# Kernel tuning notes

Measured on AMD Instinct MI355X. Metric: run time of the kernel, lower is better.

The kernel has to match this reference:

```python
import jax, jax.numpy as jnp
import numpy as np

N = 100_000   # num nodes
E = 1_600_000 # num edges (before self-loops)
IN = 128      # in_channels (FEATURE_DIM)
H = 64        # hidden_channels (HIDDEN_DIM)
NEG_SLOPE = 0.2


def setup_inputs() -> dict:
    key = jax.random.key(0)
    ks = jax.random.split(key, 8)
    s = 0.05
    return {
        "x": jax.random.normal(ks[0], (N, IN), jnp.float32),
        "edge_index": jax.random.randint(ks[1], (2, E), 0, N, jnp.int32),
        "W_gat": jax.random.normal(ks[2], (IN, H), jnp.float32) * s,
        "att_src": jax.random.normal(ks[3], (H,), jnp.float32) * s,
        "att_dst": jax.random.normal(ks[4], (H,), jnp.float32) * s,
        "b_gat": jnp.zeros((H,), jnp.float32),
        "W1": jax.random.normal(ks[5], (H, H), jnp.float32) * s,
        "b1": jnp.zeros((H,), jnp.float32),
        "W2": jax.random.normal(ks[6], (H, H), jnp.float32) * s,
        "b2": jnp.zeros((H,), jnp.float32),
    }


def _add_self_loops(src, dst, n):
    loop = jnp.arange(n, dtype=src.dtype)
    return jnp.concatenate([src, loop]), jnp.concatenate([dst, loop])


def _segment_softmax(e, seg, n):
    # numerically stable softmax over edges grouped by target node
    m = jax.ops.segment_max(e, seg, num_segments=n)
    m = jnp.where(jnp.isfinite(m), m, 0.0)  # empty segments
    ex = jnp.exp(e - m[seg])
    s = jax.ops.segment_sum(ex, seg, num_segments=n)
    return ex / (s[seg] + 1e-16)


def gat_conv(x, W, a_src, a_dst, b, src, dst, n):
    # PyG GATConv, heads=1: h = xW; e_ij = LeakyReLU(a_s.h_j + a_d.h_i)
    h = x @ W                                   # [N,H]
    alpha_s = h @ a_src                         # [N]
    alpha_d = h @ a_dst                         # [N]
    e = jax.nn.leaky_relu(alpha_s[src] + alpha_d[dst], NEG_SLOPE)  # [E]
    alpha = _segment_softmax(e, dst, n)         # [E]
    out = jax.ops.segment_sum(alpha[:, None] * h[src], dst, num_segments=n)
    return out + b


def gcn_conv(x, W, b, src, dst, n):
    # PyG GCNConv: symmetric normalization D^-1/2 A D^-1/2 (self-loops already added)
    h = x @ W                                   # [N,H]
    deg = jax.ops.segment_sum(jnp.ones(src.shape, h.dtype), dst, num_segments=n)
    dinv = jnp.where(deg > 0, jax.lax.rsqrt(deg), 0.0)
    norm = dinv[src] * dinv[dst]                # [E]
    out = jax.ops.segment_sum(norm[:, None] * h[src], dst, num_segments=n)
    return out + b


def reference(x, edge_index, W_gat, att_src, att_dst, b_gat, W1, b1, W2, b2):
    n = x.shape[0]
    src, dst = _add_self_loops(edge_index[0], edge_index[1], n)
    h = jax.nn.relu(gat_conv(x, W_gat, att_src, att_dst, b_gat, src, dst, n))
    h = jax.nn.relu(gcn_conv(h, W1, b1, src, dst, n))
    h = gcn_conv(h, W2, b2, src, dst, n)
    return h
```

## Files before the change

kernel.cpp:

```cpp
#include <hip/hip_runtime.h>
#include <hip/hip_bf16.h>
#include <math.h>

#define IN_CH 128
#define H_CH  64
#define PBLK  256
#define PTHR  512
#define BKT   256
#define MAXBK 400

typedef __attribute__((ext_vector_type(8))) short bf16x8;
typedef __attribute__((ext_vector_type(4))) float f32x4;


__device__ inline float bflo(unsigned u) { return __uint_as_float(u << 16); }
__device__ inline float bfhi(unsigned u) { return __uint_as_float(u & 0xffff0000u); }
__device__ inline unsigned short f2bf(float f) {
    unsigned x = __float_as_uint(f);
    return (unsigned short)((x + 0x7fffu + ((x >> 16) & 1u)) >> 16);
}
__device__ inline bf16x8 pack8(float4 lo, float4 hi) {
    union { bf16x8 v; unsigned short u[8]; } r;
    r.u[0] = f2bf(lo.x); r.u[1] = f2bf(lo.y); r.u[2] = f2bf(lo.z); r.u[3] = f2bf(lo.w);
    r.u[4] = f2bf(hi.x); r.u[5] = f2bf(hi.y); r.u[6] = f2bf(hi.z); r.u[7] = f2bf(hi.w);
    return r.v;
}
__device__ inline float dot8(float4 a0, float4 a1, float4 b0, float4 b1) {
    return a0.x * b0.x + a0.y * b0.y + a0.z * b0.z + a0.w * b0.w
         + a1.x * b1.x + a1.y * b1.y + a1.z * b1.z + a1.w * b1.w;
}


__global__ __launch_bounds__(PTHR) void passA(const int* __restrict__ ei, int E, int n,
                                              int nbk, int* __restrict__ blkhist) {
    __shared__ int hist[MAXBK];
    int tot = E + n;
    int CH = (tot + gridDim.x - 1) / gridDim.x;
    int beg = blockIdx.x * CH, end = min(tot, beg + CH);
    for (int k = threadIdx.x; k < nbk; k += blockDim.x) hist[k] = 0;
    __syncthreads();
    for (int idx = beg + threadIdx.x; idx < end; idx += blockDim.x) {
        int d = (idx < E) ? ei[E + idx] : (idx - E);
        atomicAdd(&hist[d >> 8], 1);
    }
    __syncthreads();
    for (int k = threadIdx.x; k < nbk; k += blockDim.x)
        blkhist[(size_t)blockIdx.x * nbk + k] = hist[k];
}

__global__ __launch_bounds__(PBLK) void passB1(const int* __restrict__ blkhist,
                                               int* __restrict__ blkbase,
                                               int* __restrict__ btot, int nbk) {
    __shared__ int sh[PBLK];
    int k = blockIdx.x, t = threadIdx.x;
    int v = blkhist[(size_t)t * nbk + k];
    sh[t] = v;
    __syncthreads();
    for (int off = 1; off < PBLK; off <<= 1) {
        int x = (t >= off) ? sh[t - off] : 0;
        __syncthreads();
        sh[t] += x;
        __syncthreads();
    }
    blkbase[(size_t)t * nbk + k] = sh[t] - v;
    if (t == PBLK - 1) btot[k] = sh[PBLK - 1];
}

__global__ __launch_bounds__(512) void passB2(const int* __restrict__ btot,
                                              int* __restrict__ bbase, int nbk, int tot) {
    __shared__ int sh[512];
    int t = threadIdx.x;
    int v = (t < nbk) ? btot[t] : 0;
    sh[t] = v;
    __syncthreads();
    for (int off = 1; off < 512; off <<= 1) {
        int x = (t >= off) ? sh[t - off] : 0;
        __syncthreads();
        sh[t] += x;
        __syncthreads();
    }
    if (t < nbk) bbase[t] = sh[t] - v;
    if (t == 0) bbase[nbk] = tot;
}

__global__ __launch_bounds__(PTHR) void passC(const int* __restrict__ ei, int E, int n, int nbk,
                                              const int* __restrict__ bbase,
                                              const int* __restrict__ blkbase,
                                              int2* __restrict__ pairs) {
    __shared__ int cur[MAXBK];
    int tot = E + n;
    int CH = (tot + gridDim.x - 1) / gridDim.x;
    int beg = blockIdx.x * CH, end = min(tot, beg + CH);
    for (int k = threadIdx.x; k < nbk; k += blockDim.x)
        cur[k] = bbase[k] + blkbase[(size_t)blockIdx.x * nbk + k];
    __syncthreads();
    for (int idx = beg + threadIdx.x; idx < end; idx += blockDim.x) {
        int s, d;
        if (idx < E) { s = ei[idx]; d = ei[E + idx]; }
        else         { s = idx - E; d = idx - E; }
        int pos = atomicAdd(&cur[d >> 8], 1);
        pairs[pos] = make_int2(s, d);
    }
}

__global__ __launch_bounds__(BKT) void passD(const int2* __restrict__ pairs,
                                             const int* __restrict__ bbase, int n, int nbk, int EP,
                                             int* __restrict__ esrc, int* __restrict__ offsets,
                                             float* __restrict__ dinv) {
    __shared__ int cnt[BKT];
    __shared__ int sh[BKT];
    __shared__ int cur[BKT];
    int k = blockIdx.x;
    int nbeg = k << 8;
    int t = threadIdx.x;
    int ebeg = bbase[k], eend = bbase[k + 1];
    cnt[t] = 0;
    __syncthreads();
    for (int e = ebeg + t; e < eend; e += BKT) {
        int2 p = pairs[e];
        atomicAdd(&cnt[p.y - nbeg], 1);
    }
    __syncthreads();
    int v = cnt[t];
    sh[t] = v;
    __syncthreads();
    for (int off = 1; off < BKT; off <<= 1) {
        int x = (t >= off) ? sh[t - off] : 0;
        __syncthreads();
        sh[t] += x;
        __syncthreads();
    }
    int lp = sh[t] - v;
    cur[t] = lp;
    int gn = nbeg + t;
    if (gn < n) {
        offsets[gn] = ebeg + lp;
        dinv[gn] = rsqrtf((float)v);
    }
    __syncthreads();
    for (int e = ebeg + t; e < eend; e += BKT) {
        int2 p = pairs[e];
        int pos = ebeg + atomicAdd(&cur[p.y - nbeg], 1);
        esrc[pos] = p.x;
    }
    if (k == 0 && t == 0) offsets[n] = EP;
}


__global__ void wprep(const float* __restrict__ W, const float* __restrict__ as,
                      const float* __restrict__ ad, float* __restrict__ w_as,
                      float* __restrict__ w_ad, int K) {
    int k = blockIdx.x * blockDim.x + threadIdx.x;
    if (k < K) {
        float s = 0.f, d = 0.f;
        for (int c = 0; c < H_CH; c++) {
            float w = W[(size_t)k * H_CH + c];
            s += w * as[c];
            d += w * ad[c];
        }
        w_as[k] = s;
        w_ad[k] = d;
    }
}


template <int K, bool GAT, bool OUTBF, bool BIASF, typename TIN>
__global__ __launch_bounds__(256) void mfma_gemm(const TIN* __restrict__ X,
                                                 const float* __restrict__ W,
                                                 void* __restrict__ outv,
                                                 const float* __restrict__ w_as,
                                                 const float* __restrict__ w_ad,
                                                 float* __restrict__ alpha_s,
                                                 float* __restrict__ alpha_d,
                                                 const float* __restrict__ bias, int n) {
    constexpr int KF = K / 32;
    int lane = threadIdx.x & 63;
    int wid  = threadIdx.x >> 6;
    int col  = lane & 15;
    int grp  = lane >> 4;

    bf16x8 bfr[KF][4];
#pragma unroll
    for (int kf = 0; kf < KF; kf++) {
        int kb = 32 * kf + 8 * grp;
#pragma unroll
        for (int cf = 0; cf < 4; cf++) {
            float w0[8];
#pragma unroll
            for (int e = 0; e < 8; e++)
                w0[e] = W[(size_t)(kb + e) * H_CH + 16 * cf + col];
            bfr[kf][cf] = pack8(make_float4(w0[0], w0[1], w0[2], w0[3]),
                                make_float4(w0[4], w0[5], w0[6], w0[7]));
        }
    }
    float bb[4] = {0.f, 0.f, 0.f, 0.f};
    if (BIASF) {
#pragma unroll
        for (int cf = 0; cf < 4; cf++) bb[cf] = bias[16 * cf + col];
    }

    int gw = blockIdx.x * (blockDim.x >> 6) + wid;
    int nw = gridDim.x * (blockDim.x >> 6);
    int ns = (n + 15) >> 4;
    for (int s = gw; s < ns; s += nw) {
        int r0 = s << 4;
        int r  = r0 + col;
        const TIN* xr = X + (size_t)(r < n ? r : 0) * K;
        bf16x8 afr[KF];
        float ps = 0.f, pd = 0.f;
#pragma unroll
        for (int kf = 0; kf < KF; kf++) {
            int kb = 32 * kf + 8 * grp;
            if constexpr (sizeof(TIN) == 2) {
                afr[kf] = *(const bf16x8*)(xr + kb);
            } else {
                float4 x0 = *(const float4*)(xr + kb);
                float4 x1 = *(const float4*)(xr + kb + 4);
                if (GAT) {
                    float4 s0 = *(const float4*)(w_as + kb);
                    float4 s1 = *(const float4*)(w_as + kb + 4);
                    float4 d0 = *(const float4*)(w_ad + kb);
                    float4 d1 = *(const float4*)(w_ad + kb + 4);
                    ps += dot8(x0, x1, s0, s1);
                    pd += dot8(x0, x1, d0, d1);
                }
                afr[kf] = pack8(x0, x1);
            }
        }
        f32x4 acc[4];
#pragma unroll
        for (int cf = 0; cf < 4; cf++) {
            acc[cf] = (f32x4){0.f, 0.f, 0.f, 0.f};
#pragma unroll
            for (int kf = 0; kf < KF; kf++)
                acc[cf] = __builtin_amdgcn_mfma_f32_16x16x32_bf16(afr[kf], bfr[kf][cf],
                                                                  acc[cf], 0, 0, 0);
        }
#pragma unroll
        for (int cf = 0; cf < 4; cf++) {
            int cc = 16 * cf + col;
#pragma unroll
            for (int g = 0; g < 4; g++) {
                int rr = r0 + 4 * grp + g;
                if (rr < n) {
                    float v = acc[cf][g] + bb[cf];
                    if (OUTBF) ((unsigned short*)outv)[(size_t)rr * H_CH + cc] = f2bf(v);
                    else       ((float*)outv)[(size_t)rr * H_CH + cc] = v;
                }
            }
        }
        if (GAT) {
            ps += __shfl_xor(ps, 16, 64); ps += __shfl_xor(ps, 32, 64);
            pd += __shfl_xor(pd, 16, 64); pd += __shfl_xor(pd, 32, 64);
            if (grp == 0 && r < n) { alpha_s[r] = ps; alpha_d[r] = pd; }
        }
    }
}


__global__ __launch_bounds__(256) void gat_gather(const unsigned short* __restrict__ h,
                                                  const int* __restrict__ offs,
                                                  const int* __restrict__ esrc,
                                                  const float* __restrict__ as,
                                                  const float* __restrict__ ad,
                                                  const float* __restrict__ bias,
                                                  unsigned short* __restrict__ out, int n) {
    __shared__ int2 sh[4][64];
    int lane = threadIdx.x & 63;
    int wid  = threadIdx.x >> 6;
    int q = lane >> 4, c = lane & 15;
    int gw = (blockIdx.x * blockDim.x + threadIdx.x) >> 6;
    int nw = (gridDim.x * blockDim.x) >> 6;
    float4 bv = *(const float4*)(bias + 4 * c);
    for (int i = gw; i < n; i += nw) {
        int beg = offs[i], end = offs[i + 1];
        float adi = ad[i];
        float a0 = 0.f, a1 = 0.f, a2 = 0.f, a3 = 0.f, s = 0.f;
        for (int base = beg; base < end; base += 64) {
            int l = base + lane;
            int sj = 0; float p = 0.f;
            if (l < end) {
                sj = esrc[l];
                float a = as[sj] + adi;
                float ev = a > 0.f ? a : 0.2f * a;
                p = __expf(ev);
            }
            sh[wid][lane] = make_int2(sj, __float_as_int(p));
            int cnt = min(64, end - base);
            int k = 0;
            for (; k + 16 <= cnt; k += 16) {
                int2 t0 = sh[wid][k + q];
                int2 t1 = sh[wid][k + 4 + q];
                int2 t2 = sh[wid][k + 8 + q];
                int2 t3 = sh[wid][k + 12 + q];
                float p0 = __int_as_float(t0.y), p1 = __int_as_float(t1.y);
                float p2 = __int_as_float(t2.y), p3 = __int_as_float(t3.y);
                uint2 u0 = *(const uint2*)(h + (size_t)t0.x * H_CH + 4 * c);
                uint2 u1 = *(const uint2*)(h + (size_t)t1.x * H_CH + 4 * c);
                uint2 u2 = *(const uint2*)(h + (size_t)t2.x * H_CH + 4 * c);
                uint2 u3 = *(const uint2*)(h + (size_t)t3.x * H_CH + 4 * c);
                a0 += p0 * bflo(u0.x); a1 += p0 * bfhi(u0.x);
                a2 += p0 * bflo(u0.y); a3 += p0 * bfhi(u0.y);
                a0 += p1 * bflo(u1.x); a1 += p1 * bfhi(u1.x);
                a2 += p1 * bflo(u1.y); a3 += p1 * bfhi(u1.y);
                a0 += p2 * bflo(u2.x); a1 += p2 * bfhi(u2.x);
                a2 += p2 * bflo(u2.y); a3 += p2 * bfhi(u2.y);
                a0 += p3 * bflo(u3.x); a1 += p3 * bfhi(u3.x);
                a2 += p3 * bflo(u3.y); a3 += p3 * bfhi(u3.y);
                s += p0 + p1 + p2 + p3;
            }
            for (; k < cnt; k += 4) {
                int2 t0 = sh[wid][k + q];
                float p0 = __int_as_float(t0.y);
                uint2 u0 = *(const uint2*)(h + (size_t)t0.x * H_CH + 4 * c);
                a0 += p0 * bflo(u0.x); a1 += p0 * bfhi(u0.x);
                a2 += p0 * bflo(u0.y); a3 += p0 * bfhi(u0.y);
                s += p0;
            }
        }
        a0 += __shfl_xor(a0, 16, 64); a0 += __shfl_xor(a0, 32, 64);
        a1 += __shfl_xor(a1, 16, 64); a1 += __shfl_xor(a1, 32, 64);
        a2 += __shfl_xor(a2, 16, 64); a2 += __shfl_xor(a2, 32, 64);
        a3 += __shfl_xor(a3, 16, 64); a3 += __shfl_xor(a3, 32, 64);
        s  += __shfl_xor(s, 16, 64);  s  += __shfl_xor(s, 32, 64);
        float invs = 1.f / (s + 1e-16f);
        if (q == 0) {
            ushort4 o;
            o.x = f2bf(fmaxf(a0 * invs + bv.x, 0.f));
            o.y = f2bf(fmaxf(a1 * invs + bv.y, 0.f));
            o.z = f2bf(fmaxf(a2 * invs + bv.z, 0.f));
            o.w = f2bf(fmaxf(a3 * invs + bv.w, 0.f));
            *(ushort4*)(out + (size_t)i * H_CH + 4 * c) = o;
        }
    }
}


template <bool RELU, bool BIASF>
__global__ __launch_bounds__(256) void gcn_gather(const unsigned short* __restrict__ h,
                                                  const int* __restrict__ offs,
                                                  const int* __restrict__ esrc,
                                                  const float* __restrict__ dinv,
                                                  const float* __restrict__ bias,
                                                  unsigned short* __restrict__ out, int n) {
    __shared__ int2 sh[4][64];
    int lane = threadIdx.x & 63;
    int wid  = threadIdx.x >> 6;
    int q = lane >> 4, c = lane & 15;
    int gw = (blockIdx.x * blockDim.x + threadIdx.x) >> 6;
    int nw = (gridDim.x * blockDim.x) >> 6;
    float4 bv = make_float4(0.f, 0.f, 0.f, 0.f);
    if (BIASF) bv = *(const float4*)(bias + 4 * c);
    for (int i = gw; i < n; i += nw) {
        int beg = offs[i], end = offs[i + 1];
        float a0 = 0.f, a1 = 0.f, a2 = 0.f, a3 = 0.f;
        for (int base = beg; base < end; base += 64) {
            int l = base + lane;
            int sj = 0; float wl = 0.f;
            if (l < end) { sj = esrc[l]; wl = dinv[sj]; }
            sh[wid][lane] = make_int2(sj, __float_as_int(wl));
            int cnt = min(64, end - base);
            int k = 0;
            for (; k + 16 <= cnt; k += 16) {
                int2 t0 = sh[wid][k + q];
                int2 t1 = sh[wid][k + 4 + q];
                int2 t2 = sh[wid][k + 8 + q];
                int2 t3 = sh[wid][k + 12 + q];
                float p0 = __int_as_float(t0.y), p1 = __int_as_float(t1.y);
                float p2 = __int_as_float(t2.y), p3 = __int_as_float(t3.y);
                uint2 u0 = *(const uint2*)(h + (size_t)t0.x * H_CH + 4 * c);
                uint2 u1 = *(const uint2*)(h + (size_t)t1.x * H_CH + 4 * c);
                uint2 u2 = *(const uint2*)(h + (size_t)t2.x * H_CH + 4 * c);
                uint2 u3 = *(const uint2*)(h + (size_t)t3.x * H_CH + 4 * c);
                a0 += p0 * bflo(u0.x); a1 += p0 * bfhi(u0.x);
                a2 += p0 * bflo(u0.y); a3 += p0 * bfhi(u0.y);
                a0 += p1 * bflo(u1.x); a1 += p1 * bfhi(u1.x);
                a2 += p1 * bflo(u1.y); a3 += p1 * bfhi(u1.y);
                a0 += p2 * bflo(u2.x); a1 += p2 * bfhi(u2.x);
                a2 += p2 * bflo(u2.y); a3 += p2 * bfhi(u2.y);
                a0 += p3 * bflo(u3.x); a1 += p3 * bfhi(u3.x);
                a2 += p3 * bflo(u3.y); a3 += p3 * bfhi(u3.y);
            }
            for (; k < cnt; k += 4) {
                int2 t0 = sh[wid][k + q];
                float p0 = __int_as_float(t0.y);
                uint2 u0 = *(const uint2*)(h + (size_t)t0.x * H_CH + 4 * c);
                a0 += p0 * bflo(u0.x); a1 += p0 * bfhi(u0.x);
                a2 += p0 * bflo(u0.y); a3 += p0 * bfhi(u0.y);
            }
        }
        a0 += __shfl_xor(a0, 16, 64); a0 += __shfl_xor(a0, 32, 64);
        a1 += __shfl_xor(a1, 16, 64); a1 += __shfl_xor(a1, 32, 64);
        a2 += __shfl_xor(a2, 16, 64); a2 += __shfl_xor(a2, 32, 64);
        a3 += __shfl_xor(a3, 16, 64); a3 += __shfl_xor(a3, 32, 64);
        float di = dinv[i];
        if (q == 0) {
            float v0 = a0 * di + bv.x, v1 = a1 * di + bv.y;
            float v2 = a2 * di + bv.z, v3 = a3 * di + bv.w;
            if (RELU) {
                v0 = fmaxf(v0, 0.f); v1 = fmaxf(v1, 0.f);
                v2 = fmaxf(v2, 0.f); v3 = fmaxf(v3, 0.f);
            }
            ushort4 o;
            o.x = f2bf(v0); o.y = f2bf(v1); o.z = f2bf(v2); o.w = f2bf(v3);
            *(ushort4*)(out + (size_t)i * H_CH + 4 * c) = o;
        }
    }
}


extern "C" void kernel_launch(void* const* d_in, const int* in_sizes, int n_in,
                              void* d_out, int out_size, void* d_ws, size_t ws_size,
                              hipStream_t stream) {
    const float* x       = (const float*)d_in[0];
    const int*   ei      = (const int*)d_in[1];
    const float* W_gat   = (const float*)d_in[2];
    const float* att_src = (const float*)d_in[3];
    const float* att_dst = (const float*)d_in[4];
    const float* b_gat   = (const float*)d_in[5];
    const float* W1      = (const float*)d_in[6];
    const float* b1      = (const float*)d_in[7];
    const float* W2      = (const float*)d_in[8];
    const float* b2      = (const float*)d_in[9];
    float* out = (float*)d_out;

    const int N  = in_sizes[0] / IN_CH;
    const int E  = in_sizes[1] / 2;
    const int EP = E + N;
    const int NBK = (N + BKT - 1) / BKT;

    char* p = (char*)d_ws;
    auto alloc = [&](size_t bytes) -> void* {
        void* r = (void*)p;
        p += (bytes + 255) & ~(size_t)255;
        return r;
    };
    unsigned short* hbf  = (unsigned short*)alloc((size_t)N * H_CH * 2);
    unsigned short* hbfA = (unsigned short*)alloc((size_t)N * H_CH * 2);
    unsigned short* hbf2 = (unsigned short*)alloc((size_t)N * H_CH * 2);
    float* alpha_s = (float*)alloc((size_t)N * 4);
    float* alpha_d = (float*)alloc((size_t)N * 4);
    float* dinv    = (float*)alloc((size_t)N * 4);
    float* w_as_g  = (float*)alloc((size_t)IN_CH * 4);
    float* w_ad_g  = (float*)alloc((size_t)IN_CH * 4);
    int*   offsets = (int*)alloc((size_t)(N + 1) * 4);
    int*   esrc    = (int*)alloc((size_t)EP * 4);
    int2*  pairs   = (int2*)alloc((size_t)EP * 8);
    int*   blkhist = (int*)alloc((size_t)PBLK * NBK * 4);
    int*   blkbase = (int*)alloc((size_t)PBLK * NBK * 4);
    int*   btot    = (int*)alloc((size_t)(NBK + 1) * 4);
    int*   bbase   = (int*)alloc((size_t)(NBK + 1) * 4);

    wprep<<<1, 128, 0, stream>>>(W_gat, att_src, att_dst, w_as_g, w_ad_g, IN_CH);

    passA<<<PBLK, PTHR, 0, stream>>>(ei, E, N, NBK, blkhist);
    passB1<<<NBK, PBLK, 0, stream>>>(blkhist, blkbase, btot, NBK);
    passB2<<<1, 512, 0, stream>>>(btot, bbase, NBK, EP);
    passC<<<PBLK, PTHR, 0, stream>>>(ei, E, N, NBK, bbase, blkbase, pairs);
    passD<<<NBK, BKT, 0, stream>>>(pairs, bbase, N, NBK, EP, esrc, offsets, dinv);

    mfma_gemm<IN_CH, true, true, false, float><<<512, 256, 0, stream>>>(
        x, W_gat, hbf, w_as_g, w_ad_g, alpha_s, alpha_d, nullptr, N);
    gat_gather<<<2048, 256, 0, stream>>>(hbf, offsets, esrc, alpha_s, alpha_d, b_gat, hbfA, N);

    mfma_gemm<H_CH, false, true, false, unsigned short><<<512, 256, 0, stream>>>(
        hbfA, W1, hbf, nullptr, nullptr, nullptr, nullptr, nullptr, N);
    gcn_gather<true, true><<<2048, 256, 0, stream>>>(hbf, offsets, esrc, dinv, b1, hbf2, N);

    gcn_gather<false, false><<<2048, 256, 0, stream>>>(hbf2, offsets, esrc, dinv, nullptr,
                                                       hbfA, N);
    mfma_gemm<H_CH, false, false, true, unsigned short><<<512, 256, 0, stream>>>(
        hbfA, W2, out, nullptr, nullptr, nullptr, nullptr, b2, N);
}
```

Before: 205.6 us.

## Fold scan and weight-prep kernels into consumers and simplify gather loops

Removes the passB2 bucket-base scan kernel by recomputing the scan redundantly inside each passC block and a per-block reduction inside passD. The wprep kernel is also dropped, with the attention-projected weights computed per block in shared memory inside the GAT GEMM. Both changes cut kernel launches and serial dependencies. The GAT and GCN gather loops no longer stage indices and weights through LDS; each lane loads 4 consecutive edge indices directly, at the cost of redundant index and weight loads and extra per-block setup work.

```diff
diff --git a/kernel.cpp b/kernel.cpp
--- a/kernel.cpp
+++ b/kernel.cpp
@@ -28,6 +28,9 @@
 __device__ inline float dot8(float4 a0, float4 a1, float4 b0, float4 b1) {
     return a0.x * b0.x + a0.y * b0.y + a0.z * b0.z + a0.w * b0.w
          + a1.x * b1.x + a1.y * b1.y + a1.z * b1.z + a1.w * b1.w;
+}
+__device__ inline float leakyexp(float a) {
+    return __expf(a > 0.f ? a : 0.2f * a);
 }
 
 
@@ -66,35 +69,29 @@
     if (t == PBLK - 1) btot[k] = sh[PBLK - 1];
 }
 
-__global__ __launch_bounds__(512) void passB2(const int* __restrict__ btot,
-                                              int* __restrict__ bbase, int nbk, int tot) {
-    __shared__ int sh[512];
-    int t = threadIdx.x;
-    int v = (t < nbk) ? btot[t] : 0;
-    sh[t] = v;
-    __syncthreads();
-    for (int off = 1; off < 512; off <<= 1) {
-        int x = (t >= off) ? sh[t - off] : 0;
-        __syncthreads();
-        sh[t] += x;
-        __syncthreads();
-    }
-    if (t < nbk) bbase[t] = sh[t] - v;
-    if (t == 0) bbase[nbk] = tot;
-}
-
 __global__ __launch_bounds__(PTHR) void passC(const int* __restrict__ ei, int E, int n, int nbk,
-                                              const int* __restrict__ bbase,
+                                              const int* __restrict__ btot,
                                               const int* __restrict__ blkbase,
                                               int2* __restrict__ pairs) {
     __shared__ int cur[MAXBK];
+    __shared__ int sc[PTHR];
+    int t = threadIdx.x;
+    int v = (t < nbk) ? btot[t] : 0;
+    sc[t] = v;
+    __syncthreads();
+    for (int off = 1; off < PTHR; off <<= 1) {
+        int x = (t >= off) ? sc[t - off] : 0;
+        __syncthreads();
+        sc[t] += x;
+        __syncthreads();
+    }
+    if (t < nbk) cur[t] = (sc[t] - v) + blkbase[(size_t)blockIdx.x * nbk + t];
+    __syncthreads();
+
     int tot = E + n;
     int CH = (tot + gridDim.x - 1) / gridDim.x;
     int beg = blockIdx.x * CH, end = min(tot, beg + CH);
-    for (int k = threadIdx.x; k < nbk; k += blockDim.x)
-        cur[k] = bbase[k] + blkbase[(size_t)blockIdx.x * nbk + k];
-    __syncthreads();
-    for (int idx = beg + threadIdx.x; idx < end; idx += blockDim.x) {
+    for (int idx = beg + t; idx < end; idx += blockDim.x) {
         int s, d;
         if (idx < E) { s = ei[idx]; d = ei[E + idx]; }
         else         { s = idx - E; d = idx - E; }
@@ -104,16 +101,28 @@
 }
 
 __global__ __launch_bounds__(BKT) void passD(const int2* __restrict__ pairs,
-                                             const int* __restrict__ bbase, int n, int nbk, int EP,
+                                             const int* __restrict__ btot, int n, int nbk, int EP,
                                              int* __restrict__ esrc, int* __restrict__ offsets,
                                              float* __restrict__ dinv) {
     __shared__ int cnt[BKT];
     __shared__ int sh[BKT];
     __shared__ int cur[BKT];
+    __shared__ int red[BKT];
     int k = blockIdx.x;
     int nbeg = k << 8;
     int t = threadIdx.x;
-    int ebeg = bbase[k], eend = bbase[k + 1];
+
+    int part = 0;
+    for (int j = t; j < k; j += BKT) part += btot[j];
+    red[t] = part;
+    __syncthreads();
+    for (int off = BKT / 2; off; off >>= 1) {
+        if (t < off) red[t] += red[t + off];
+        __syncthreads();
+    }
+    int ebeg = red[0];
+    int eend = ebeg + btot[k];
+
     cnt[t] = 0;
     __syncthreads();
     for (int e = ebeg + t; e < eend; e += BKT) {
@@ -147,33 +156,32 @@
 }
 
 
-__global__ void wprep(const float* __restrict__ W, const float* __restrict__ as,
-                      const float* __restrict__ ad, float* __restrict__ w_as,
-                      float* __restrict__ w_ad, int K) {
-    int k = blockIdx.x * blockDim.x + threadIdx.x;
-    if (k < K) {
-        float s = 0.f, d = 0.f;
-        for (int c = 0; c < H_CH; c++) {
-            float w = W[(size_t)k * H_CH + c];
-            s += w * as[c];
-            d += w * ad[c];
-        }
-        w_as[k] = s;
-        w_ad[k] = d;
-    }
-}
-
-
 template <int K, bool GAT, bool OUTBF, bool BIASF, typename TIN>
 __global__ __launch_bounds__(256) void mfma_gemm(const TIN* __restrict__ X,
                                                  const float* __restrict__ W,
                                                  void* __restrict__ outv,
-                                                 const float* __restrict__ w_as,
-                                                 const float* __restrict__ w_ad,
+                                                 const float* __restrict__ att_s,
+                                                 const float* __restrict__ att_d,
                                                  float* __restrict__ alpha_s,
                                                  float* __restrict__ alpha_d,
                                                  const float* __restrict__ bias, int n) {
     constexpr int KF = K / 32;
+    __shared__ __align__(16) float swas[K];
+    __shared__ __align__(16) float swad[K];
+    if (GAT) {
+        if (threadIdx.x < K) {
+            float s = 0.f, d = 0.f;
+            for (int cc = 0; cc < H_CH; cc++) {
+                float w = W[(size_t)threadIdx.x * H_CH + cc];
+                s += w * att_s[cc];
+                d += w * att_d[cc];
+            }
+            swas[threadIdx.x] = s;
+            swad[threadIdx.x] = d;
+        }
+        __syncthreads();
+    }
+
     int lane = threadIdx.x & 63;
     int wid  = threadIdx.x >> 6;
     int col  = lane & 15;
@@ -217,10 +225,10 @@
                 float4 x0 = *(const float4*)(xr + kb);
                 float4 x1 = *(const float4*)(xr + kb + 4);
                 if (GAT) {
-                    float4 s0 = *(const float4*)(w_as + kb);
-                    float4 s1 = *(const float4*)(w_as + kb + 4);
-                    float4 d0 = *(const float4*)(w_ad + kb);
-                    float4 d1 = *(const float4*)(w_ad + kb + 4);
+                    float4 s0 = *(const float4*)(swas + kb);
+                    float4 s1 = *(const float4*)(swas + kb + 4);
+                    float4 d0 = *(const float4*)(swad + kb);
+                    float4 d1 = *(const float4*)(swad + kb + 4);
                     ps += dot8(x0, x1, s0, s1);
                     pd += dot8(x0, x1, d0, d1);
                 }
@@ -265,9 +273,7 @@
                                                   const float* __restrict__ ad,
                                                   const float* __restrict__ bias,
                                                   unsigned short* __restrict__ out, int n) {
-    __shared__ int2 sh[4][64];
     int lane = threadIdx.x & 63;
-    int wid  = threadIdx.x >> 6;
     int q = lane >> 4, c = lane & 15;
     int gw = (blockIdx.x * blockDim.x + threadIdx.x) >> 6;
     int nw = (gridDim.x * blockDim.x) >> 6;
@@ -276,47 +282,38 @@
         int beg = offs[i], end = offs[i + 1];
         float adi = ad[i];
         float a0 = 0.f, a1 = 0.f, a2 = 0.f, a3 = 0.f, s = 0.f;
-        for (int base = beg; base < end; base += 64) {
-            int l = base + lane;
-            int sj = 0; float p = 0.f;
-            if (l < end) {
-                sj = esrc[l];
-                float a = as[sj] + adi;
-                float ev = a > 0.f ? a : 0.2f * a;
-                p = __expf(ev);
-            }
-            sh[wid][lane] = make_int2(sj, __float_as_int(p));
-            int cnt = min(64, end - base);
-            int k = 0;
-            for (; k + 16 <= cnt; k += 16) {
-                int2 t0 = sh[wid][k + q];
-                int2 t1 = sh[wid][k + 4 + q];
-                int2 t2 = sh[wid][k + 8 + q];
-                int2 t3 = sh[wid][k + 12 + q];
-                float p0 = __int_as_float(t0.y), p1 = __int_as_float(t1.y);
-                float p2 = __int_as_float(t2.y), p3 = __int_as_float(t3.y);
-                uint2 u0 = *(const uint2*)(h + (size_t)t0.x * H_CH + 4 * c);
-                uint2 u1 = *(const uint2*)(h + (size_t)t1.x * H_CH + 4 * c);
-                uint2 u2 = *(const uint2*)(h + (size_t)t2.x * H_CH + 4 * c);
-                uint2 u3 = *(const uint2*)(h + (size_t)t3.x * H_CH + 4 * c);
-                a0 += p0 * bflo(u0.x); a1 += p0 * bfhi(u0.x);
-                a2 += p0 * bflo(u0.y); a3 += p0 * bfhi(u0.y);
-                a0 += p1 * bflo(u1.x); a1 += p1 * bfhi(u1.x);
-                a2 += p1 * bflo(u1.y); a3 += p1 * bfhi(u1.y);
-                a0 += p2 * bflo(u2.x); a1 += p2 * bfhi(u2.x);
-                a2 += p2 * bflo(u2.y); a3 += p2 * bfhi(u2.y);
-                a0 += p3 * bflo(u3.x); a1 += p3 * bfhi(u3.x);
-                a2 += p3 * bflo(u3.y); a3 += p3 * bfhi(u3.y);
-                s += p0 + p1 + p2 + p3;
-            }
-            for (; k < cnt; k += 4) {
-                int2 t0 = sh[wid][k + q];
-                float p0 = __int_as_float(t0.y);
-                uint2 u0 = *(const uint2*)(h + (size_t)t0.x * H_CH + 4 * c);
-                a0 += p0 * bflo(u0.x); a1 += p0 * bfhi(u0.x);
-                a2 += p0 * bflo(u0.y); a3 += p0 * bfhi(u0.y);
-                s += p0;
-            }
+        int k = beg;
+#pragma unroll 2
+        for (; k + 16 <= end; k += 16) {
+            int e = k + 4 * q;
+            int s0 = esrc[e], s1 = esrc[e + 1], s2 = esrc[e + 2], s3 = esrc[e + 3];
+            float p0 = leakyexp(as[s0] + adi);
+            float p1 = leakyexp(as[s1] + adi);
+            float p2 = leakyexp(as[s2] + adi);
+            float p3 = leakyexp(as[s3] + adi);
+            uint2 u0 = *(const uint2*)(h + (size_t)s0 * H_CH + 4 * c);
+            uint2 u1 = *(const uint2*)(h + (size_t)s1 * H_CH + 4 * c);
+            uint2 u2 = *(const uint2*)(h + (size_t)s2 * H_CH + 4 * c);
+            uint2 u3 = *(const uint2*)(h + (size_t)s3 * H_CH + 4 * c);
+            a0 += p0 * bflo(u0.x); a1 += p0 * bfhi(u0.x);
+            a2 += p0 * bflo(u0.y); a3 += p0 * bfhi(u0.y);
+            a0 += p1 * bflo(u1.x); a1 += p1 * bfhi(u1.x);
+            a2 += p1 * bflo(u1.y); a3 += p1 * bfhi(u1.y);
+            a0 += p2 * bflo(u2.x); a1 += p2 * bfhi(u2.x);
+            a2 += p2 * bflo(u2.y); a3 += p2 * bfhi(u2.y);
+            a0 += p3 * bflo(u3.x); a1 += p3 * bfhi(u3.x);
+            a2 += p3 * bflo(u3.y); a3 += p3 * bfhi(u3.y);
+            s += p0 + p1 + p2 + p3;
+        }
+        for (; k < end; k += 4) {
+            int e = k + q;
+            bool vld = e < end;
+            int sj = esrc[vld ? e : end - 1];
+            float p = vld ? leakyexp(as[sj] + adi) : 0.f;
+            uint2 u = *(const uint2*)(h + (size_t)sj * H_CH + 4 * c);
+            a0 += p * bflo(u.x); a1 += p * bfhi(u.x);
+            a2 += p * bflo(u.y); a3 += p * bfhi(u.y);
+            s += p;
         }
         a0 += __shfl_xor(a0, 16, 64); a0 += __shfl_xor(a0, 32, 64);
         a1 += __shfl_xor(a1, 16, 64); a1 += __shfl_xor(a1, 32, 64);
@@ -343,9 +340,7 @@
                                                   const float* __restrict__ dinv,
                                                   const float* __restrict__ bias,
                                                   unsigned short* __restrict__ out, int n) {
-    __shared__ int2 sh[4][64];
     int lane = threadIdx.x & 63;
-    int wid  = threadIdx.x >> 6;
     int q = lane >> 4, c = lane & 15;
     int gw = (blockIdx.x * blockDim.x + threadIdx.x) >> 6;
     int nw = (gridDim.x * blockDim.x) >> 6;
@@ -354,40 +349,33 @@
     for (int i = gw; i < n; i += nw) {
         int beg = offs[i], end = offs[i + 1];
         float a0 = 0.f, a1 = 0.f, a2 = 0.f, a3 = 0.f;
-        for (int base = beg; base < end; base += 64) {
-            int l = base + lane;
-            int sj = 0; float wl = 0.f;
-            if (l < end) { sj = esrc[l]; wl = dinv[sj]; }
-            sh[wid][lane] = make_int2(sj, __float_as_int(wl));
-            int cnt = min(64, end - base);
-            int k = 0;
-            for (; k + 16 <= cnt; k += 16) {
-                int2 t0 = sh[wid][k + q];
-                int2 t1 = sh[wid][k + 4 + q];
-                int2 t2 = sh[wid][k + 8 + q];
-                int2 t3 = sh[wid][k + 12 + q];
-                float p0 = __int_as_float(t0.y), p1 = __int_as_float(t1.y);
-                float p2 = __int_as_float(t2.y), p3 = __int_as_float(t3.y);
-                uint2 u0 = *(const uint2*)(h + (size_t)t0.x * H_CH + 4 * c);
-                uint2 u1 = *(const uint2*)(h + (size_t)t1.x * H_CH + 4 * c);
-                uint2 u2 = *(const uint2*)(h + (size_t)t2.x * H_CH + 4 * c);
-                uint2 u3 = *(const uint2*)(h + (size_t)t3.x * H_CH + 4 * c);
-                a0 += p0 * bflo(u0.x); a1 += p0 * bfhi(u0.x);
-                a2 += p0 * bflo(u0.y); a3 += p0 * bfhi(u0.y);
-                a0 += p1 * bflo(u1.x); a1 += p1 * bfhi(u1.x);
-                a2 += p1 * bflo(u1.y); a3 += p1 * bfhi(u1.y);
-                a0 += p2 * bflo(u2.x); a1 += p2 * bfhi(u2.x);
-                a2 += p2 * bflo(u2.y); a3 += p2 * bfhi(u2.y);
-                a0 += p3 * bflo(u3.x); a1 += p3 * bfhi(u3.x);
-                a2 += p3 * bflo(u3.y); a3 += p3 * bfhi(u3.y);
-            }
-            for (; k < cnt; k += 4) {
-                int2 t0 = sh[wid][k + q];
-                float p0 = __int_as_float(t0.y);
-                uint2 u0 = *(const uint2*)(h + (size_t)t0.x * H_CH + 4 * c);
-                a0 += p0 * bflo(u0.x); a1 += p0 * bfhi(u0.x);
-                a2 += p0 * bflo(u0.y); a3 += p0 * bfhi(u0.y);
-            }
+        int k = beg;
+#pragma unroll 2
+        for (; k + 16 <= end; k += 16) {
+            int e = k + 4 * q;
+            int s0 = esrc[e], s1 = esrc[e + 1], s2 = esrc[e + 2], s3 = esrc[e + 3];
+            float w0 = dinv[s0], w1 = dinv[s1], w2 = dinv[s2], w3 = dinv[s3];
+            uint2 u0 = *(const uint2*)(h + (size_t)s0 * H_CH + 4 * c);
+            uint2 u1 = *(const uint2*)(h + (size_t)s1 * H_CH + 4 * c);
+            uint2 u2 = *(const uint2*)(h + (size_t)s2 * H_CH + 4 * c);
+            uint2 u3 = *(const uint2*)(h + (size_t)s3 * H_CH + 4 * c);
+            a0 += w0 * bflo(u0.x); a1 += w0 * bfhi(u0.x);
+            a2 += w0 * bflo(u0.y); a3 += w0 * bfhi(u0.y);
+            a0 += w1 * bflo(u1.x); a1 += w1 * bfhi(u1.x);
+            a2 += w1 * bflo(u1.y); a3 += w1 * bfhi(u1.y);
+            a0 += w2 * bflo(u2.x); a1 += w2 * bfhi(u2.x);
+            a2 += w2 * bflo(u2.y); a3 += w2 * bfhi(u2.y);
+            a0 += w3 * bflo(u3.x); a1 += w3 * bfhi(u3.x);
+            a2 += w3 * bflo(u3.y); a3 += w3 * bfhi(u3.y);
+        }
+        for (; k < end; k += 4) {
+            int e = k + q;
+            bool vld = e < end;
+            int sj = esrc[vld ? e : end - 1];
+            float w = vld ? dinv[sj] : 0.f;
+            uint2 u = *(const uint2*)(h + (size_t)sj * H_CH + 4 * c);
+            a0 += w * bflo(u.x); a1 += w * bfhi(u.x);
+            a2 += w * bflo(u.y); a3 += w * bfhi(u.y);
         }
         a0 += __shfl_xor(a0, 16, 64); a0 += __shfl_xor(a0, 32, 64);
         a1 += __shfl_xor(a1, 16, 64); a1 += __shfl_xor(a1, 32, 64);
@@ -441,26 +429,20 @@
     float* alpha_s = (float*)alloc((size_t)N * 4);
     float* alpha_d = (float*)alloc((size_t)N * 4);
     float* dinv    = (float*)alloc((size_t)N * 4);
-    float* w_as_g  = (float*)alloc((size_t)IN_CH * 4);
-    float* w_ad_g  = (float*)alloc((size_t)IN_CH * 4);
     int*   offsets = (int*)alloc((size_t)(N + 1) * 4);
     int*   esrc    = (int*)alloc((size_t)EP * 4);
     int2*  pairs   = (int2*)alloc((size_t)EP * 8);
     int*   blkhist = (int*)alloc((size_t)PBLK * NBK * 4);
     int*   blkbase = (int*)alloc((size_t)PBLK * NBK * 4);
     int*   btot    = (int*)alloc((size_t)(NBK + 1) * 4);
-    int*   bbase   = (int*)alloc((size_t)(NBK + 1) * 4);
-
-    wprep<<<1, 128, 0, stream>>>(W_gat, att_src, att_dst, w_as_g, w_ad_g, IN_CH);
 
     passA<<<PBLK, PTHR, 0, stream>>>(ei, E, N, NBK, blkhist);
     passB1<<<NBK, PBLK, 0, stream>>>(blkhist, blkbase, btot, NBK);
-    passB2<<<1, 512, 0, stream>>>(btot, bbase, NBK, EP);
-    passC<<<PBLK, PTHR, 0, stream>>>(ei, E, N, NBK, bbase, blkbase, pairs);
-    passD<<<NBK, BKT, 0, stream>>>(pairs, bbase, N, NBK, EP, esrc, offsets, dinv);
+    passC<<<PBLK, PTHR, 0, stream>>>(ei, E, N, NBK, btot, blkbase, pairs);
+    passD<<<NBK, BKT, 0, stream>>>(pairs, btot, N, NBK, EP, esrc, offsets, dinv);
 
     mfma_gemm<IN_CH, true, true, false, float><<<512, 256, 0, stream>>>(
-        x, W_gat, hbf, w_as_g, w_ad_g, alpha_s, alpha_d, nullptr, N);
+        x, W_gat, hbf, att_src, att_dst, alpha_s, alpha_d, nullptr, N);
     gat_gather<<<2048, 256, 0, stream>>>(hbf, offsets, esrc, alpha_s, alpha_d, b_gat, hbfA, N);
 
     mfma_gemm<H_CH, false, true, false, unsigned short><<<512, 256, 0, stream>>>(
```

Result: slower. 306.4 us (+49.0%).
